# Performance work log

Measured on AMD Instinct MI355X. Metric: run time of the kernel, lower is better.

## Reference

```python
import jax, jax.numpy as jnp
import numpy as np

# Dims: B INRs, N probe points, d_in=2 coords, hidden H, out D_OUT, proj P
B, N, D_IN, H, D_OUT, P = 128, 4096, 2, 128, 3, 128
W0_SIREN = 30.0  # SIREN frequency scale
LN_EPS = 1e-5


def setup_inputs() -> dict:
    key = jax.random.key(0)
    ks = jax.random.split(key, 12)
    sn = lambda k, shape, sc: (jax.random.normal(k, shape, dtype=jnp.float32) * sc)
    return {
        # per-sample SIREN params, torch layout: weight [b, in, out, 1], bias [b, out, 1]
        "w0": sn(ks[0], (B, D_IN, H, 1), 1.0 / D_IN),
        "w1": sn(ks[1], (B, H, H, 1), np.sqrt(6.0 / H) / W0_SIREN),
        "w2": sn(ks[2], (B, H, D_OUT, 1), np.sqrt(6.0 / H) / W0_SIREN),
        "b0": sn(ks[3], (B, H, 1), 0.1),
        "b1": sn(ks[4], (B, H, 1), 0.1),
        "b2": sn(ks[5], (B, D_OUT, 1), 0.1),
        # learned probe coordinates, initialized U[-1, 1) as in the module
        "inputs": jax.random.uniform(ks[6], (1, N, D_IN), dtype=jnp.float32, minval=-1.0, maxval=1.0),
        # projection (num_inputs -> proj_dim) + LayerNorm params, one per probed layer (4 total)
        "pw": sn(ks[7], (4, N, P), 1.0 / np.sqrt(N)),
        "pb": jnp.zeros((4, P), jnp.float32),
        "ln_g": jnp.ones((4, P), jnp.float32),
        "ln_b": jnp.zeros((4, P), jnp.float32),
    }


def _layernorm(x, g, b):
    m = jnp.mean(x, axis=-1, keepdims=True)
    v = jnp.mean(jnp.square(x - m), axis=-1, keepdims=True)
    return (x - m) * jax.lax.rsqrt(v + LN_EPS) * g + b


def reference(w0, w1, w2, b0, b1, b2, inputs, pw, pb, ln_g, ln_b):
    b = w0.shape[0]
    x = jnp.broadcast_to(inputs, (b,) + inputs.shape[1:])  # [b, n, d_in]

    def lin(h, W, bb):
        # per-sample linear: [b,n,i] @ [b,i,o] + [b,1,o]
        return jnp.einsum('bni,bio->bno', h, W[..., 0]) + bb[:, None, :, 0]

    h1 = jnp.sin(W0_SIREN * lin(x, w0, b0))   # [b, n, H]
    h2 = jnp.sin(W0_SIREN * lin(h1, w1, b1))  # [b, n, H]
    h3 = lin(h2, w2, b2)                      # [b, n, D_OUT] (last layer: no sine)
    feats = [x, h1, h2, h3]  # probe features per node layer (input coords + activations)

    outs = []
    for i, f in enumerate(feats):
        # permute to [b, dim_i, n], project n -> P, then LayerNorm over P
        z = jnp.einsum('bnd,np->bdp', f, pw[i]) + pb[i]
        outs.append(_layernorm(z, ln_g[i], ln_b[i]))
    return jnp.concatenate(outs, axis=1)  # [b, d_in + H + H + D_OUT, P]
```

## Files before the change

### kernel.cpp

```cpp
#include <hip/hip_runtime.h>
#include <hip/hip_bf16.h>


typedef unsigned short u16;
typedef __attribute__((ext_vector_type(8))) short short8;
typedef __attribute__((ext_vector_type(4))) short short4v;
typedef __attribute__((ext_vector_type(4))) float f32x4;
typedef __attribute__((ext_vector_type(4))) float float4v;

#define DEV __device__ __forceinline__

#define KSC 4.7746482927568605f

DEV float b2f(u16 h){ return __uint_as_float(((unsigned)h) << 16); }
DEV u16 f2b(float f){
  unsigned u = __float_as_uint(f);
  return (u16)((u + 0x7FFFu + ((u >> 16) & 1u)) >> 16);
}
DEV u16 f2b_hw(float f){
  __hip_bfloat16 h = __float2bfloat16(f);
  return __builtin_bit_cast(unsigned short, h);
}
DEV float sin_rev(float r){
#if __has_builtin(__builtin_amdgcn_sinf)
  return __builtin_amdgcn_sinf(r);
#else
  return __sinf(r * 6.283185307179586f);
#endif
}

DEV int is_bf16_fmt(const void* lng){ return *(const unsigned*)lng == 0x3F803F80u; }
struct In {
  const float* f; const u16* h; int bf;
  DEV In(const void* p, int b_) : f((const float*)p), h((const u16*)p), bf(b_) {}
  DEV float at(size_t i) const { return bf ? b2f(h[i]) : f[i]; }
};

__global__ __launch_bounds__(256) void k_prep(const void* pwv, const void* inpv,
                                              const void* lngv,
                                              u16* __restrict__ pwT2,
                                              float* __restrict__ xbuf,
                                              float* __restrict__ zpart){
  const int bf = is_bf16_fmt(lngv);
  const int t = threadIdx.x;
  if (blockIdx.x == 256){
    In inp(inpv, bf);
    for (int i = t; i < 8192; i += 256) xbuf[i] = inp.at(i);
    return;
  }
  In pw(pwv, bf);
  const int layer = blockIdx.x >> 6;
  const int nc = blockIdx.x & 63;
  const int n0 = nc * 64;

  if (layer == 0){
    In inp(inpv, bf);
    const int d = t >> 7, p = t & 127;
    float s = 0.f;
#pragma unroll 8
    for (int k = 0; k < 64; k++)
      s = fmaf(inp.at((size_t)(n0 + k) * 2 + d),
               pw.at((size_t)(n0 + k) * 128 + p), s);
    zpart[(size_t)nc * 384 + d * 128 + p] = s;
    return;
  }

  __shared__ u16 tile[64 * 129];
  const size_t base = ((size_t)layer * 4096 + n0) * 128;
#pragma unroll
  for (int k = 0; k < 32; k++){
    int idx = k * 256 + t, n = idx >> 7, p = idx & 127;
    tile[n * 129 + p] = f2b(pw.at(base + (size_t)n * 128 + p));
  }
  if (layer == 3 && t < 128){
    float s = 0.f;
#pragma unroll 8
    for (int k = 0; k < 64; k++)
      s += pw.at(base + (size_t)k * 128 + t);
    zpart[(size_t)nc * 384 + 256 + t] = s;
  }
  __syncthreads();
  u16* dst = pwT2 + ((size_t)(layer - 1) * 128 + nc * 2) * 4096;
#pragma unroll
  for (int k = 0; k < 32; k++){
    int o = k * 256 + t;
    int frag = (o >> 3) & 511, j = o & 7;
    int p = ((frag >> 6) << 4) | ((frag >> 2) & 15);
    int nn = ((o >> 12) << 5) | ((frag & 3) << 3) | j;
    dst[o] = tile[nn * 129 + p];
  }
}

#define S_NK 136
#define S_T  40

__global__ __launch_bounds__(512, 2)
void k_main(const void* w0v, const void* w1v, const void* w2v,
            const void* b0v, const void* b1v, const void* lgv,
            const u16* __restrict__ pwTg, const float* __restrict__ xbuf,
            float* __restrict__ outp, int TS){
  __shared__ __align__(16) u16 sh1nk[32 * S_NK];
  __shared__ __align__(16) u16 sh1T[128 * S_T];
  __shared__ __align__(16) u16 sh2T[2][128 * S_T];
  __shared__ float sW2[512];

  float* sZ3 = (float*)sh1nk;

  const int bf = is_bf16_fmt(lgv);
  In w0(w0v, bf), w1(w1v, bf), w2(w2v, bf), b0(b0v, bf), b1(b1v, bf);

  const int t = threadIdx.x;
  const int b = blockIdx.x & 127, sseg = blockIdx.x >> 7;
  const int lane = t & 63, wave = t >> 6, quad = lane >> 4, r16 = lane & 15;
  const int wr = wave >> 2, wc = wave & 3;

  if (t >= 256 && t < 384){
    int i = t - 256;
    sW2[i * 4 + 0] = w2.at(((size_t)b * 128 + i) * 3 + 0);
    sW2[i * 4 + 1] = w2.at(((size_t)b * 128 + i) * 3 + 1);
    sW2[i * 4 + 2] = w2.at(((size_t)b * 128 + i) * 3 + 2);
    sW2[i * 4 + 3] = 0.f;
  }

  const int p1n = t >> 4, p1hb = (t & 15) * 8;
  float w00[8], w01[8], b00[8];
#pragma unroll
  for (int j = 0; j < 8; j++){
    w00[j] = w0.at((size_t)b * 256 + p1hb + j) * KSC;
    w01[j] = w0.at((size_t)b * 256 + 128 + p1hb + j) * KSC;
    b00[j] = b0.at((size_t)b * 128 + p1hb + j) * KSC;
  }
  const int p2h = t & 127, p2nb = (t >> 7) * 8;
  const float q00 = w0.at((size_t)b * 256 + p2h) * KSC;
  const float q01 = w0.at((size_t)b * 256 + 128 + p2h) * KSC;
  const float qb0 = b0.at((size_t)b * 128 + p2h) * KSC;
  const int hA = wc * 32 + r16, hB = wc * 32 + 16 + r16;
  const float bias1kA = b1.at((size_t)b * 128 + hA) * KSC;
  const float bias1kB = b1.at((size_t)b * 128 + hB) * KSC;

  short8 w1f[4][2];
#pragma unroll
  for (int ks = 0; ks < 4; ks++){
#pragma unroll
    for (int j = 0; j < 8; j++){
      w1f[ks][0][j] = (short)f2b(w1.at((size_t)b * 16384 +
                                    (size_t)(ks * 32 + quad * 8 + j) * 128 + hA));
      w1f[ks][1][j] = (short)f2b(w1.at((size_t)b * 16384 +
                                    (size_t)(ks * 32 + quad * 8 + j) * 128 + hB));
    }
  }

  const u16* bsrc0 = pwTg + (size_t)((wc * 2    ) * 64 + r16 * 4 + quad) * 8;
  const u16* bsrc1 = pwTg + (size_t)((wc * 2 + 1) * 64 + r16 * 4 + quad) * 8;

  const f32x4 zz = {0.f,0.f,0.f,0.f};
  f32x4 az1[8], az2[8], ay[8];
#pragma unroll
  for (int i = 0; i < 8; i++){ az1[i] = zz; az2[i] = zz; ay[i] = zz; }

  const int nb0 = sseg * TS;
  short8 bbc[3][2];
#pragma unroll
  for (int L = 0; L < 3; L++){
    bbc[L][0] = *(const short8*)(bsrc0 + ((size_t)L * 128 + nb0) * 4096);
    bbc[L][1] = *(const short8*)(bsrc1 + ((size_t)L * 128 + nb0) * 4096);
  }
  short8 bb2p0 = bbc[1][0], bb2p1 = bbc[1][1];
  short8 bb3p0 = bbc[2][0], bb3p1 = bbc[2][1];
  float2 xp1 = *(const float2*)(xbuf + (size_t)(nb0 * 32 + p1n) * 2);

  __syncthreads();

  int cb = 0;
  for (int nt = 0; nt < TS; nt++){
    const int n0 = (sseg * TS + nt) * 32;

    float4v xq[4];
#pragma unroll
    for (int q = 0; q < 4; q++)
      xq[q] = *(const float4v*)(xbuf + (size_t)(n0 + p2nb) * 2 + q * 4);
    {
      short8 v;
#pragma unroll
      for (int j = 0; j < 8; j++){
        float a = fmaf(xp1.y, w01[j], fmaf(xp1.x, w00[j], b00[j]));
        a -= rintf(a);
        v[j] = (short)f2b_hw(sin_rev(a));
      }
      *(short8*)&sh1nk[p1n * S_NK + p1hb] = v;
    }
    {
      short8 v;
#pragma unroll
      for (int j = 0; j < 8; j++){
        float x0 = xq[j >> 1][(j & 1) * 2], x1 = xq[j >> 1][(j & 1) * 2 + 1];
        float a = fmaf(x1, q01, fmaf(x0, q00, qb0));
        a -= rintf(a);
        v[j] = (short)f2b_hw(sin_rev(a));
      }
      *(short8*)&sh1T[p2h * S_T + p2nb] = v;
    }
    if (nt){
      const u16* s2p = sh2T[cb ^ 1];
#pragma unroll
      for (int m = 0; m < 4; m++){
        short8 a = *(const short8*)&s2p[(wr * 64 + m * 16 + r16) * S_T + quad * 8];
        az2[m*2+0] = __builtin_amdgcn_mfma_f32_16x16x32_bf16(a, bb2p0, az2[m*2+0], 0, 0, 0);
        az2[m*2+1] = __builtin_amdgcn_mfma_f32_16x16x32_bf16(a, bb2p1, az2[m*2+1], 0, 0, 0);
        ay[m*2+0]  = __builtin_amdgcn_mfma_f32_16x16x32_bf16(a, bb3p0, ay[m*2+0], 0, 0, 0);
        ay[m*2+1]  = __builtin_amdgcn_mfma_f32_16x16x32_bf16(a, bb3p1, ay[m*2+1], 0, 0, 0);
      }
    }
    __syncthreads();

    {
      const int nn = (nt + 1 < TS) ? nt + 1 : nt;
      const int nbn = sseg * TS + nn;
      short8 bbn[3][2];
#pragma unroll
      for (int L = 0; L < 3; L++){
        bbn[L][0] = *(const short8*)(bsrc0 + ((size_t)L * 128 + nbn) * 4096);
        bbn[L][1] = *(const short8*)(bsrc1 + ((size_t)L * 128 + nbn) * 4096);
      }
      float2 xp1n = *(const float2*)(xbuf + (size_t)(nbn * 32 + p1n) * 2);

      f32x4 h0 = zz, h1a = zz;
#pragma unroll
      for (int ks = 0; ks < 4; ks++){
        short8 a = *(short8*)&sh1nk[(wr * 16 + r16) * S_NK + ks * 32 + quad * 8];
        h0  = __builtin_amdgcn_mfma_f32_16x16x32_bf16(a, w1f[ks][0], h0, 0, 0, 0);
        h1a = __builtin_amdgcn_mfma_f32_16x16x32_bf16(a, w1f[ks][1], h1a, 0, 0, 0);
      }
#pragma unroll
      for (int m = 0; m < 4; m++){
        short8 a = *(const short8*)&sh1T[(wr * 64 + m * 16 + r16) * S_T + quad * 8];
        az1[m*2+0] = __builtin_amdgcn_mfma_f32_16x16x32_bf16(a, bbc[0][0], az1[m*2+0], 0, 0, 0);
        az1[m*2+1] = __builtin_amdgcn_mfma_f32_16x16x32_bf16(a, bbc[0][1], az1[m*2+1], 0, 0, 0);
      }
      {
        short4v v;
#pragma unroll
        for (int r = 0; r < 4; r++){
          float a = fmaf(h0[r], KSC, bias1kA); a -= rintf(a);
          v[r] = (short)f2b_hw(sin_rev(a));
        }
        *(short4v*)&sh2T[cb][hA * S_T + wr * 16 + quad * 4] = v;
#pragma unroll
        for (int r = 0; r < 4; r++){
          float a = fmaf(h1a[r], KSC, bias1kB); a -= rintf(a);
          v[r] = (short)f2b_hw(sin_rev(a));
        }
        *(short4v*)&sh2T[cb][hB * S_T + wr * 16 + quad * 4] = v;
      }

      bb2p0 = bbc[1][0]; bb2p1 = bbc[1][1];
      bb3p0 = bbc[2][0]; bb3p1 = bbc[2][1];
#pragma unroll
      for (int L = 0; L < 3; L++){ bbc[L][0] = bbn[L][0]; bbc[L][1] = bbn[L][1]; }
      xp1 = xp1n;
    }
    __syncthreads();
    cb ^= 1;
  }

  {
    const u16* s2p = sh2T[cb ^ 1];
#pragma unroll
    for (int m = 0; m < 4; m++){
      short8 a = *(const short8*)&s2p[(wr * 64 + m * 16 + r16) * S_T + quad * 8];
      az2[m*2+0] = __builtin_amdgcn_mfma_f32_16x16x32_bf16(a, bb2p0, az2[m*2+0], 0, 0, 0);
      az2[m*2+1] = __builtin_amdgcn_mfma_f32_16x16x32_bf16(a, bb2p1, az2[m*2+1], 0, 0, 0);
      ay[m*2+0]  = __builtin_amdgcn_mfma_f32_16x16x32_bf16(a, bb3p0, ay[m*2+0], 0, 0, 0);
      ay[m*2+1]  = __builtin_amdgcn_mfma_f32_16x16x32_bf16(a, bb3p1, ay[m*2+1], 0, 0, 0);
    }
  }

  float z3p[3][2];
#pragma unroll
  for (int dd = 0; dd < 3; dd++){
#pragma unroll
    for (int n = 0; n < 2; n++){
      float a = 0.f;
#pragma unroll
      for (int m = 0; m < 4; m++)
#pragma unroll
        for (int r = 0; r < 4; r++)
          a = fmaf(sW2[(wr * 64 + m * 16 + quad * 4 + r) * 4 + dd], ay[m*2+n][r], a);
      a += __shfl_xor(a, 16, 64); a += __shfl_xor(a, 32, 64);
      z3p[dd][n] = a;
    }
  }
  if (lane < 16){
#pragma unroll
    for (int dd = 0; dd < 3; dd++)
#pragma unroll
      for (int n = 0; n < 2; n++)
        sZ3[((wr * 4 + wc) * 3 + dd) * 32 + n * 16 + r16] = z3p[dd][n];
  }

  float* zp = outp + ((size_t)(sseg * 128 + b)) * 261 * 128;
#pragma unroll
  for (int m = 0; m < 4; m++)
#pragma unroll
    for (int n = 0; n < 2; n++)
#pragma unroll
      for (int r = 0; r < 4; r++){
        int drow = wr * 64 + m * 16 + quad * 4 + r;
        int pcol = wc * 32 + n * 16 + r16;
        zp[(size_t)(2 + drow) * 128 + pcol]   = az1[m*2+n][r];
        zp[(size_t)(130 + drow) * 128 + pcol] = az2[m*2+n][r];
      }
  __syncthreads();
  if (t < 384){
    int dd = t >> 7, p = t & 127, wcc = p >> 5, pl = p & 31;
    float v = sZ3[((0 * 4 + wcc) * 3 + dd) * 32 + pl]
            + sZ3[((1 * 4 + wcc) * 3 + dd) * 32 + pl];
    zp[(size_t)(258 + dd) * 128 + p] = v;
  }
}

__global__ __launch_bounds__(256)
void k_ln(const float* __restrict__ zp, const void* pbv, const void* lgv,
          const void* lbv, const void* b2v, const float* __restrict__ zpart,
          float* __restrict__ out, int split){
  const int bf = is_bf16_fmt(lgv);
  In pb(pbv, bf), lg(lgv, bf), lb(lbv, bf), b2(b2v, bf);
  const int lane = threadIdx.x & 63;
  const int row = blockIdx.x * 4 + (threadIdx.x >> 6);
  const int b = row / 261, d = row % 261;
  const int grp = (d < 2) ? 0 : (d < 130) ? 1 : (d < 258) ? 2 : 3;
  const int p0 = lane * 2;
  float v0 = pb.at(grp * 128 + p0), v1 = pb.at(grp * 128 + p0 + 1);
  if (d < 2){
    float s0 = 0.f, s1z = 0.f;
    for (int c = 0; c < 64; c++){
      s0  += zpart[(size_t)c * 384 + d * 128 + p0];
      s1z += zpart[(size_t)c * 384 + d * 128 + p0 + 1];
    }
    v0 += s0;
    v1 += s1z;
  } else {
    for (int s2 = 0; s2 < split; s2++){
      const float* zr = zp + ((size_t)(s2 * 128 + b) * 261 + d) * 128;
      v0 += zr[p0]; v1 += zr[p0 + 1];
    }
    if (d >= 258){
      float s0 = 0.f, s1z = 0.f;
      for (int c = 0; c < 64; c++){
        s0  += zpart[(size_t)c * 384 + 256 + p0];
        s1z += zpart[(size_t)c * 384 + 256 + p0 + 1];
      }
      float bb = b2.at((size_t)b * 3 + (d - 258));
      v0 = fmaf(bb, s0, v0);
      v1 = fmaf(bb, s1z, v1);
    }
  }
  float s1 = v0 + v1, s2s = v0 * v0 + v1 * v1;
#pragma unroll
  for (int o = 1; o < 64; o <<= 1){
    s1 += __shfl_xor(s1, o, 64);
    s2s += __shfl_xor(s2s, o, 64);
  }
  float m = s1 * (1.f / 128.f);
  float var = fmaf(-m, m, s2s * (1.f / 128.f));
  float inv = rsqrtf(fmaxf(var, 0.f) + 1e-5f);
  float2 o2;
  o2.x = (v0 - m) * inv * lg.at(grp * 128 + p0)     + lb.at(grp * 128 + p0);
  o2.y = (v1 - m) * inv * lg.at(grp * 128 + p0 + 1) + lb.at(grp * 128 + p0 + 1);
  *(float2*)(out + (size_t)row * 128 + p0) = o2;
}

extern "C" void kernel_launch(void* const* d_in, const int* in_sizes, int n_in,
                              void* d_out, int out_size, void* d_ws, size_t ws_size,
                              hipStream_t stream){
  const void* w0  = d_in[0];
  const void* w1  = d_in[1];
  const void* w2  = d_in[2];
  const void* b0  = d_in[3];
  const void* b1  = d_in[4];
  const void* b2  = d_in[5];
  const void* inp = d_in[6];
  const void* pw  = d_in[7];
  const void* pb  = d_in[8];
  const void* lng = d_in[9];
  const void* lnb = d_in[10];
  float* out = (float*)d_out;

  char* ws = (char*)d_ws;
  u16* pwT2    = (u16*)ws;
  float* xbuf  = (float*)(ws + 3145728);
  float* zpart = (float*)(ws + 3145728 + 32768);
  const size_t zoff = 3145728 + 32768 + 98304;
  float* zp = (float*)(ws + zoff);
  const size_t seg = (size_t)128 * 261 * 128 * 4;

  const int split = (ws_size >= zoff + 2 * seg) ? 2 : 1;

  k_prep<<<257, 256, 0, stream>>>(pw, inp, lng, pwT2, xbuf, zpart);
  k_main<<<128 * split, 512, 0, stream>>>(w0, w1, w2, b0, b1,
      lng, pwT2, xbuf, zp, 4096 / (32 * split));
  k_ln<<<(128 * 261) / 4, 256, 0, stream>>>(zp, pb, lng, lnb, b2, zpart, out, split);
}
```

Measured before the change: 228.4 us.

## Double-buffer layer-1 tiles to drop one barrier per iteration

Adds double buffers for the layer-1 activation tiles (sh1nk and sh1T). Each iteration now computes the sine activations for tile nt+1 into the spare buffer while the MFMAs consume tile nt, and a prologue fills the first buffer. This removes one __syncthreads per tile and moves the coordinate loads two tiles ahead. In exchange the kernel uses more LDS, which could reduce occupancy, and keeps more values in registers.

```diff
diff --git a/kernel.cpp b/kernel.cpp
--- a/kernel.cpp
+++ b/kernel.cpp
@@ -99,8 +99,8 @@
             const void* b0v, const void* b1v, const void* lgv,
             const u16* __restrict__ pwTg, const float* __restrict__ xbuf,
             float* __restrict__ outp, int TS){
-  __shared__ __align__(16) u16 sh1nk[32 * S_NK];
-  __shared__ __align__(16) u16 sh1T[128 * S_T];
+  __shared__ __align__(16) u16 sh1nk[2][32 * S_NK];
+  __shared__ __align__(16) u16 sh1T[2][128 * S_T];
   __shared__ __align__(16) u16 sh2T[2][128 * S_T];
   __shared__ float sW2[512];
 
@@ -167,18 +167,40 @@
   }
   short8 bb2p0 = bbc[1][0], bb2p1 = bbc[1][1];
   short8 bb3p0 = bbc[2][0], bb3p1 = bbc[2][1];
-  float2 xp1 = *(const float2*)(xbuf + (size_t)(nb0 * 32 + p1n) * 2);
+
+  {
+    float2 x0 = *(const float2*)(xbuf + (size_t)(nb0 * 32 + p1n) * 2);
+    short8 v;
+#pragma unroll
+    for (int j = 0; j < 8; j++){
+      float a = fmaf(x0.y, w01[j], fmaf(x0.x, w00[j], b00[j]));
+      a -= rintf(a);
+      v[j] = (short)f2b_hw(sin_rev(a));
+    }
+    *(short8*)&sh1nk[0][p1n * S_NK + p1hb] = v;
+    float4v xa;
+#pragma unroll
+    for (int j = 0; j < 8; j++){
+      if ((j & 1) == 0)
+        xa = *(const float4v*)(xbuf + (size_t)(nb0 * 32 + p2nb) * 2 + (j >> 1) * 4);
+      float xx0 = xa[(j & 1) * 2], xx1 = xa[(j & 1) * 2 + 1];
+      float a = fmaf(xx1, q01, fmaf(xx0, q00, qb0));
+      a -= rintf(a);
+      v[j] = (short)f2b_hw(sin_rev(a));
+    }
+    *(short8*)&sh1T[0][p2h * S_T + p2nb] = v;
+  }
+  const int nbp1 = nb0 + ((TS > 1) ? 1 : 0);
+  float2 xp1 = *(const float2*)(xbuf + (size_t)(nbp1 * 32 + p1n) * 2);
+  float4v xqp[4];
+#pragma unroll
+  for (int q = 0; q < 4; q++)
+    xqp[q] = *(const float4v*)(xbuf + (size_t)(nbp1 * 32 + p2nb) * 2 + q * 4);
 
   __syncthreads();
 
   int cb = 0;
   for (int nt = 0; nt < TS; nt++){
-    const int n0 = (sseg * TS + nt) * 32;
-
-    float4v xq[4];
-#pragma unroll
-    for (int q = 0; q < 4; q++)
-      xq[q] = *(const float4v*)(xbuf + (size_t)(n0 + p2nb) * 2 + q * 4);
     {
       short8 v;
 #pragma unroll
@@ -187,18 +209,15 @@
         a -= rintf(a);
         v[j] = (short)f2b_hw(sin_rev(a));
       }
-      *(short8*)&sh1nk[p1n * S_NK + p1hb] = v;
-    }
-    {
-      short8 v;
+      *(short8*)&sh1nk[cb ^ 1][p1n * S_NK + p1hb] = v;
 #pragma unroll
       for (int j = 0; j < 8; j++){
-        float x0 = xq[j >> 1][(j & 1) * 2], x1 = xq[j >> 1][(j & 1) * 2 + 1];
+        float x0 = xqp[j >> 1][(j & 1) * 2], x1 = xqp[j >> 1][(j & 1) * 2 + 1];
         float a = fmaf(x1, q01, fmaf(x0, q00, qb0));
         a -= rintf(a);
         v[j] = (short)f2b_hw(sin_rev(a));
       }
-      *(short8*)&sh1T[p2h * S_T + p2nb] = v;
+      *(short8*)&sh1T[cb ^ 1][p2h * S_T + p2nb] = v;
     }
     if (nt){
       const u16* s2p = sh2T[cb ^ 1];
@@ -211,53 +230,57 @@
         ay[m*2+1]  = __builtin_amdgcn_mfma_f32_16x16x32_bf16(a, bb3p1, ay[m*2+1], 0, 0, 0);
       }
     }
-    __syncthreads();
-
     {
-      const int nn = (nt + 1 < TS) ? nt + 1 : nt;
-      const int nbn = sseg * TS + nn;
+      f32x4 h0 = zz, h1a = zz;
+#pragma unroll
+      for (int ks = 0; ks < 4; ks++){
+        short8 a = *(short8*)&sh1nk[cb][(wr * 16 + r16) * S_NK + ks * 32 + quad * 8];
+        h0  = __builtin_amdgcn_mfma_f32_16x16x32_bf16(a, w1f[ks][0], h0, 0, 0, 0);
+        h1a = __builtin_amdgcn_mfma_f32_16x16x32_bf16(a, w1f[ks][1], h1a, 0, 0, 0);
+      }
+#pragma unroll
+      for (int m = 0; m < 4; m++){
+        short8 a = *(const short8*)&sh1T[cb][(wr * 64 + m * 16 + r16) * S_T + quad * 8];
+        az1[m*2+0] = __builtin_amdgcn_mfma_f32_16x16x32_bf16(a, bbc[0][0], az1[m*2+0], 0, 0, 0);
+        az1[m*2+1] = __builtin_amdgcn_mfma_f32_16x16x32_bf16(a, bbc[0][1], az1[m*2+1], 0, 0, 0);
+      }
+      short4v v;
+#pragma unroll
+      for (int r = 0; r < 4; r++){
+        float a = fmaf(h0[r], KSC, bias1kA); a -= rintf(a);
+        v[r] = (short)f2b_hw(sin_rev(a));
+      }
+      *(short4v*)&sh2T[cb][hA * S_T + wr * 16 + quad * 4] = v;
+#pragma unroll
+      for (int r = 0; r < 4; r++){
+        float a = fmaf(h1a[r], KSC, bias1kB); a -= rintf(a);
+        v[r] = (short)f2b_hw(sin_rev(a));
+      }
+      *(short4v*)&sh2T[cb][hB * S_T + wr * 16 + quad * 4] = v;
+    }
+    {
+      const int nn  = (nt + 1 < TS) ? nt + 1 : nt;
+      const int nn2 = (nt + 2 < TS) ? nt + 2 : TS - 1;
+      const int nbn = sseg * TS + nn, nbn2 = sseg * TS + nn2;
       short8 bbn[3][2];
 #pragma unroll
       for (int L = 0; L < 3; L++){
         bbn[L][0] = *(const short8*)(bsrc0 + ((size_t)L * 128 + nbn) * 4096);
         bbn[L][1] = *(const short8*)(bsrc1 + ((size_t)L * 128 + nbn) * 4096);
       }
-      float2 xp1n = *(const float2*)(xbuf + (size_t)(nbn * 32 + p1n) * 2);
-
-      f32x4 h0 = zz, h1a = zz;
-#pragma unroll
-      for (int ks = 0; ks < 4; ks++){
-        short8 a = *(short8*)&sh1nk[(wr * 16 + r16) * S_NK + ks * 32 + quad * 8];
-        h0  = __builtin_amdgcn_mfma_f32_16x16x32_bf16(a, w1f[ks][0], h0, 0, 0, 0);
-        h1a = __builtin_amdgcn_mfma_f32_16x16x32_bf16(a, w1f[ks][1], h1a, 0, 0, 0);
-      }
-#pragma unroll
-      for (int m = 0; m < 4; m++){
-        short8 a = *(const short8*)&sh1T[(wr * 64 + m * 16 + r16) * S_T + quad * 8];
-        az1[m*2+0] = __builtin_amdgcn_mfma_f32_16x16x32_bf16(a, bbc[0][0], az1[m*2+0], 0, 0, 0);
-        az1[m*2+1] = __builtin_amdgcn_mfma_f32_16x16x32_bf16(a, bbc[0][1], az1[m*2+1], 0, 0, 0);
-      }
-      {
-        short4v v;
-#pragma unroll
-        for (int r = 0; r < 4; r++){
-          float a = fmaf(h0[r], KSC, bias1kA); a -= rintf(a);
-          v[r] = (short)f2b_hw(sin_rev(a));
-        }
-        *(short4v*)&sh2T[cb][hA * S_T + wr * 16 + quad * 4] = v;
-#pragma unroll
-        for (int r = 0; r < 4; r++){
-          float a = fmaf(h1a[r], KSC, bias1kB); a -= rintf(a);
-          v[r] = (short)f2b_hw(sin_rev(a));
-        }
-        *(short4v*)&sh2T[cb][hB * S_T + wr * 16 + quad * 4] = v;
-      }
+      float2 xp1n = *(const float2*)(xbuf + (size_t)(nbn2 * 32 + p1n) * 2);
+      float4v xqn[4];
+#pragma unroll
+      for (int q = 0; q < 4; q++)
+        xqn[q] = *(const float4v*)(xbuf + (size_t)(nbn2 * 32 + p2nb) * 2 + q * 4);
 
       bb2p0 = bbc[1][0]; bb2p1 = bbc[1][1];
       bb3p0 = bbc[2][0]; bb3p1 = bbc[2][1];
 #pragma unroll
       for (int L = 0; L < 3; L++){ bbc[L][0] = bbn[L][0]; bbc[L][1] = bbn[L][1]; }
       xp1 = xp1n;
+#pragma unroll
+      for (int q = 0; q < 4; q++) xqp[q] = xqn[q];
     }
     __syncthreads();
     cb ^= 1;
```

Measured after the change: 227.4 us. Within noise of the previous version (-0.4%).
